# Performance work log

Measured on AMD Instinct MI355X. Metric: run time of the kernel, lower is better.

The kernel has to match this reference:

```python
import jax, jax.numpy as jnp
import numpy as np

N_AGENTS = 32
STATE_DIM = 6 * N_AGENTS      # 192
CONTROL_DIM = 3 * N_AGENTS    # 96
HIDDEN = 100
NEWTON_ITERS = 40

# Index maps from the cvxpy objective:
#   p[u_x_r]^T u[u_idx] + p[u_y_r]^T u[2*u_idx] + p[u_z_r]^T u[3*u_idx]
_u_idx = np.arange(N_AGENTS)
P_IDX = np.concatenate([3 * np.arange(1, N_AGENTS + 1),
                        4 * np.arange(1, N_AGENTS + 1),
                        5 * np.arange(1, N_AGENTS + 1)])
U_IDX = np.concatenate([_u_idx, 2 * _u_idx, 3 * _u_idx])


def _p_net(t, z, W1, b1, W2, b2, W3, b3):
    # DefaultPNet: MLP on concat([t, z]) with tanh hiddens (hidden_dim=100)
    x = jnp.concatenate([t, z], axis=-1)          # [B, 1+STATE_DIM]
    h = jnp.tanh(x @ W1 + b1)
    h = jnp.tanh(h @ W2 + b2)
    return h @ W3 + b3                            # [B, STATE_DIM]


def _solve_qp(q):
    # min_u q^T u + 0.5||u||^2 + 0.25||u||^4  (unconstrained, strictly convex)
    # Stationarity: q + (1+||u||^2) u = 0 => u = -q/(1+s), s = ||u||^2
    # => s (1+s)^2 = ||q||^2 ; solve scalar cubic per row via Newton.
    r = jnp.sum(q * q, axis=-1)                   # [B]
    s0 = jnp.cbrt(r)                              # good init: s ~ r^(1/3) for large r

    def step(s, _):
        one = 1.0 + s
        f = s * one * one - r
        fp = one * one + 2.0 * s * one
        return jnp.maximum(s - f / fp, 0.0), None

    s, _ = jax.lax.scan(step, s0, None, length=NEWTON_ITERS)
    return -q / (1.0 + s)[:, None]                # [B, CONTROL_DIM]


def setup_inputs() -> dict:
    key = jax.random.key(0)
    ks = jax.random.split(key, 8)
    B = 131072
    in_dim = 1 + STATE_DIM
    sc1 = 1.0 / np.sqrt(in_dim)
    sc2 = 1.0 / np.sqrt(HIDDEN)
    return {
        "z": jax.random.normal(ks[0], (B, STATE_DIM), jnp.float32),
        "t": jax.random.uniform(ks[1], (B, 1), jnp.float32),
        "W1": jax.random.normal(ks[2], (in_dim, HIDDEN), jnp.float32) * sc1,
        "b1": jnp.zeros((HIDDEN,), jnp.float32),
        "W2": jax.random.normal(ks[3], (HIDDEN, HIDDEN), jnp.float32) * sc2,
        "b2": jnp.zeros((HIDDEN,), jnp.float32),
        "W3": jax.random.normal(ks[4], (HIDDEN, STATE_DIM), jnp.float32) * sc2,
        "b3": jnp.zeros((STATE_DIM,), jnp.float32),
    }


def reference(z, t, W1, b1, W2, b2, W3, b3):
    p = _p_net(t, z, W1, b1, W2, b2, W3, b3)      # [B, STATE_DIM]
    # Accumulate linear coefficients onto u (indices overlap, so scatter-add)
    q = jnp.zeros((p.shape[0], CONTROL_DIM), p.dtype).at[:, U_IDX].add(p[:, P_IDX])
    return _solve_qp(q)                            # ustar [B, CONTROL_DIM]
```

## Files before the change

kernel.cpp:

```cpp
#include <hip/hip_runtime.h>
#include <hip/hip_bf16.h>


typedef __attribute__((ext_vector_type(8))) short short8;
typedef __attribute__((ext_vector_type(4))) short short4v;
typedef __attribute__((ext_vector_type(4))) float f32x4;

#define HST 116

__device__ __forceinline__ unsigned short f2bf(float f) {
  unsigned u = __float_as_uint(f);
  u += 0x7fffu + ((u >> 16) & 1u);
  return (unsigned short)(u >> 16);
}
__device__ __forceinline__ float tanh_fast(float x) {
  float ax = fabsf(x);
  float e = __builtin_amdgcn_exp2f(ax * -2.88539008177792681f);
  float r = (1.f - e) * __builtin_amdgcn_rcpf(1.f + e);
  return copysignf(r, x);
}

__global__ void cvx_prep(const float* __restrict__ W1, const float* __restrict__ b1,
                         const float* __restrict__ W2, const float* __restrict__ b2,
                         const float* __restrict__ W3, const float* __restrict__ b3,
                         short* __restrict__ pw) {
  int idx = blockIdx.x * 256 + threadIdx.x;

  if (idx < 21504) {
    int kt = idx / 3584, rem = idx % 3584;
    int nt = rem / 512, e = rem % 512;
    int lane = e >> 3, j = e & 7;
    int k = kt * 32 + (lane >> 4) * 8 + j;
    int n = nt * 16 + (lane & 15);
    float wv = (n < 100) ? W1[(k + 1) * 100 + n] : 0.f;
    pw[(kt * 7 + nt) * 512 + e] = (short)f2bf(wv);
    return;
  }
  idx -= 21504;
  if (idx < 14336) {
    int kt = idx / 3584, rem = idx % 3584;
    int nt = rem / 512, e = rem % 512;
    int lane = e >> 3, j = e & 7;
    int k = kt * 32 + (lane >> 4) * 8 + j;
    int n = nt * 16 + (lane & 15);
    float wv = (k < 100 && n < 100) ? W2[k * 100 + n] : 0.f;
    pw[21504 + (kt * 7 + nt) * 512 + e] = (short)f2bf(wv);
    return;
  }
  idx -= 14336;
  if (idx < 12288) {
    int kt = idx / 3072, rem = idx % 3072;
    int nt = rem / 512, e = rem % 512;
    int lane = e >> 3, j = e & 7;
    int k = kt * 32 + (lane >> 4) * 8 + j;
    int u = nt * 16 + (lane & 15);
    float wv = 0.f;
    if (k < 100) {
      const float* wr = W3 + k * 192;
      if (u <= 31) wv += wr[3 * u + 3];
      if ((u & 1) == 0 && u <= 62) wv += wr[2 * u + 4];
      if (u % 3 == 0 && u <= 93) wv += wr[(5 * u) / 3 + 5];
    }
    pw[35840 + (kt * 6 + nt) * 512 + e] = (short)f2bf(wv);
    return;
  }
  idx -= 12288;
  float* cb = (float*)(pw + 48128);
  if (idx < 112) { cb[idx] = (idx < 100) ? W1[idx] : 0.f; return; }
  idx -= 112;
  if (idx < 112) { cb[112 + idx] = (idx < 100) ? b1[idx] : 0.f; return; }
  idx -= 112;
  if (idx < 112) { cb[224 + idx] = (idx < 100) ? b2[idx] : 0.f; return; }
  idx -= 112;
  if (idx < 96) {
    int u = idx;
    float v = 0.f;
    if (u <= 31) v += b3[3 * u + 3];
    if ((u & 1) == 0 && u <= 62) v += b3[2 * u + 4];
    if (u % 3 == 0 && u <= 93) v += b3[(5 * u) / 3 + 5];
    cb[336 + u] = v;
  }
}

__global__ __launch_bounds__(512, 2) void cvx_main(
    const float* __restrict__ zin, const float* __restrict__ tin,
    const short* __restrict__ pw, float* __restrict__ out) {
  __shared__ __align__(16) short wbuf[48128];
  __shared__ __align__(16) short hbuf[8 * 32 * HST];

  const int tid = threadIdx.x;
  const int wid = tid >> 6;
  const int lane = tid & 63;
  const int l15 = lane & 15;
  const int qd = lane >> 4;

  for (int f = wid; f < 94; f += 8) {
    const short* g = pw + f * 512 + lane * 8;
    __builtin_amdgcn_global_load_lds(
        (const __attribute__((address_space(1))) void*)g,
        (__attribute__((address_space(3))) void*)&wbuf[f * 512], 16, 0, 0);
  }

  const float* cb = (const float*)(pw + 48128);
  float w0v[7], b1v[7], b2v[7], bqv[6];
#pragma unroll
  for (int nt = 0; nt < 7; nt++) {
    w0v[nt] = cb[nt * 16 + l15];
    b1v[nt] = cb[112 + nt * 16 + l15];
    b2v[nt] = cb[224 + nt * 16 + l15];
  }
#pragma unroll
  for (int nt = 0; nt < 6; nt++) bqv[nt] = cb[336 + nt * 16 + l15];

  const int row0 = blockIdx.x * 512 + wid * 32;
  const int hb = wid * 32 * HST;

  f32x4 zc[2][6][2];
  float tc[2];
#pragma unroll
  for (int mt = 0; mt < 2; mt++) {
    const float* zr = zin + (size_t)(row0 + mt * 16 + l15) * 192 + qd * 8;
#pragma unroll
    for (int kt = 0; kt < 6; kt++) {
      zc[mt][kt][0] = *(const f32x4*)(zr + kt * 32);
      zc[mt][kt][1] = *(const f32x4*)(zr + kt * 32 + 4);
    }
    tc[mt] = tin[row0 + mt * 16 + l15];
  }

  __syncthreads();

  auto ldh = [&](int off) -> short8 {
    short4v a = *(const short4v*)&hbuf[off];
    short4v b = *(const short4v*)&hbuf[off + 4];
    return __builtin_shufflevector(a, b, 0, 1, 2, 3, 4, 5, 6, 7);
  };

#pragma unroll 1
  for (int it = 0; it < 2; ++it) {
    const int rb = row0 + it * 256;

    short8 XA[2][6];
#pragma unroll
    for (int mt = 0; mt < 2; mt++)
#pragma unroll
      for (int kt = 0; kt < 6; kt++) {
        union { short8 s; __hip_bfloat162 h[4]; } u;
        f32x4 a = zc[mt][kt][0], b = zc[mt][kt][1];
        u.h[0] = __float22bfloat162_rn(make_float2(a[0], a[1]));
        u.h[1] = __float22bfloat162_rn(make_float2(a[2], a[3]));
        u.h[2] = __float22bfloat162_rn(make_float2(b[0], b[1]));
        u.h[3] = __float22bfloat162_rn(make_float2(b[2], b[3]));
        XA[mt][kt] = u.s;
      }
    float tv0 = tc[0], tv1 = tc[1];

    if (it == 0) {
#pragma unroll
      for (int mt = 0; mt < 2; mt++) {
        const float* zr = zin + (size_t)(row0 + 256 + mt * 16 + l15) * 192 + qd * 8;
#pragma unroll
        for (int kt = 0; kt < 6; kt++) {
          zc[mt][kt][0] = *(const f32x4*)(zr + kt * 32);
          zc[mt][kt][1] = *(const f32x4*)(zr + kt * 32 + 4);
        }
        tc[mt] = tin[row0 + 256 + mt * 16 + l15];
      }
    }

    f32x4 acc[2][7];
#pragma unroll
    for (int nt = 0; nt < 7; nt++) {
      f32x4 zzz = {0.f, 0.f, 0.f, 0.f};
      acc[0][nt] = zzz; acc[1][nt] = zzz;
    }
#pragma unroll
    for (int kt = 0; kt < 6; kt++)
#pragma unroll
      for (int nt = 0; nt < 7; nt++) {
        short8 bf = *(const short8*)&wbuf[(kt * 7 + nt) * 512 + lane * 8];
        acc[0][nt] = __builtin_amdgcn_mfma_f32_16x16x32_bf16(XA[0][kt], bf, acc[0][nt], 0, 0, 0);
        acc[1][nt] = __builtin_amdgcn_mfma_f32_16x16x32_bf16(XA[1][kt], bf, acc[1][nt], 0, 0, 0);
      }
    float tr[2][4];
#pragma unroll
    for (int r = 0; r < 4; r++) {
      tr[0][r] = __shfl(tv0, qd * 4 + r);
      tr[1][r] = __shfl(tv1, qd * 4 + r);
    }
#pragma unroll
    for (int mt = 0; mt < 2; mt++)
#pragma unroll
      for (int nt = 0; nt < 7; nt++)
#pragma unroll
        for (int r = 0; r < 4; r++) {
          float v = fmaf(tr[mt][r], w0v[nt], acc[mt][nt][r] + b1v[nt]);
          hbuf[hb + (mt * 16 + qd * 4 + r) * HST + nt * 16 + l15] = (short)f2bf(tanh_fast(v));
        }

    short8 HA[2][4];
#pragma unroll
    for (int mt = 0; mt < 2; mt++) {
      int ro = hb + (mt * 16 + l15) * HST;
#pragma unroll
      for (int kt = 0; kt < 3; kt++) HA[mt][kt] = ldh(ro + kt * 32 + qd * 8);
      HA[mt][3] = ldh(ro + 96 + (qd & 1) * 8);
    }
#pragma unroll
    for (int nt = 0; nt < 7; nt++) {
      f32x4 zzz = {0.f, 0.f, 0.f, 0.f};
      acc[0][nt] = zzz; acc[1][nt] = zzz;
    }
#pragma unroll
    for (int kt = 0; kt < 4; kt++)
#pragma unroll
      for (int nt = 0; nt < 7; nt++) {
        short8 bf = *(const short8*)&wbuf[(42 + kt * 7 + nt) * 512 + lane * 8];
        acc[0][nt] = __builtin_amdgcn_mfma_f32_16x16x32_bf16(HA[0][kt], bf, acc[0][nt], 0, 0, 0);
        acc[1][nt] = __builtin_amdgcn_mfma_f32_16x16x32_bf16(HA[1][kt], bf, acc[1][nt], 0, 0, 0);
      }
#pragma unroll
    for (int mt = 0; mt < 2; mt++)
#pragma unroll
      for (int nt = 0; nt < 7; nt++)
#pragma unroll
        for (int r = 0; r < 4; r++) {
          float v = acc[mt][nt][r] + b2v[nt];
          hbuf[hb + (mt * 16 + qd * 4 + r) * HST + nt * 16 + l15] = (short)f2bf(tanh_fast(v));
        }

#pragma unroll
    for (int mt = 0; mt < 2; mt++) {
      int ro = hb + (mt * 16 + l15) * HST;
#pragma unroll
      for (int kt = 0; kt < 3; kt++) HA[mt][kt] = ldh(ro + kt * 32 + qd * 8);
      HA[mt][3] = ldh(ro + 96 + (qd & 1) * 8);
    }
    f32x4 qa[2][6];
#pragma unroll
    for (int nt = 0; nt < 6; nt++) {
      f32x4 zzz = {0.f, 0.f, 0.f, 0.f};
      qa[0][nt] = zzz; qa[1][nt] = zzz;
    }
#pragma unroll
    for (int kt = 0; kt < 4; kt++)
#pragma unroll
      for (int nt = 0; nt < 6; nt++) {
        short8 bf = *(const short8*)&wbuf[(70 + kt * 6 + nt) * 512 + lane * 8];
        qa[0][nt] = __builtin_amdgcn_mfma_f32_16x16x32_bf16(HA[0][kt], bf, qa[0][nt], 0, 0, 0);
        qa[1][nt] = __builtin_amdgcn_mfma_f32_16x16x32_bf16(HA[1][kt], bf, qa[1][nt], 0, 0, 0);
      }

#pragma unroll
    for (int mt = 0; mt < 2; mt++) {
#pragma unroll
      for (int nt = 0; nt < 6; nt++) {
        float bq = bqv[nt];
        qa[mt][nt][0] += bq; qa[mt][nt][1] += bq;
        qa[mt][nt][2] += bq; qa[mt][nt][3] += bq;
      }
      f32x4 rs = {0.f, 0.f, 0.f, 0.f};
#pragma unroll
      for (int nt = 0; nt < 6; nt++) rs += qa[mt][nt] * qa[mt][nt];
      float rv[4];
#pragma unroll
      for (int r = 0; r < 4; r++) {
        float v = rs[r];
        v += __shfl_xor(v, 1);
        v += __shfl_xor(v, 2);
        v += __shfl_xor(v, 4);
        v += __shfl_xor(v, 8);
        rv[r] = v;
      }
      float r2 = rv[l15 & 3];
      float s = __builtin_amdgcn_exp2f(__builtin_amdgcn_logf(r2) * 0.333333333333f);
#pragma unroll
      for (int itn = 0; itn < 8; itn++) {
        float one = 1.f + s;
        float fv = fmaf(s * one, one, -r2);
        float fp = one * fmaf(2.f, s, one);
        s = fmaxf(s - fv * __builtin_amdgcn_rcpf(fp), 0.f);
      }
      float myinv = -__builtin_amdgcn_rcpf(1.f + s);
#pragma unroll
      for (int r = 0; r < 4; r++) {
        float inv = __shfl(myinv, (lane & 48) | r);
        float* orow = out + (size_t)(rb + mt * 16 + qd * 4 + r) * 96;
#pragma unroll
        for (int nt = 0; nt < 6; nt++)
          orow[nt * 16 + l15] = qa[mt][nt][r] * inv;
      }
    }
  }
}

extern "C" void kernel_launch(void* const* d_in, const int* in_sizes, int n_in,
                              void* d_out, int out_size, void* d_ws, size_t ws_size,
                              hipStream_t stream) {
  const float* z  = (const float*)d_in[0];
  const float* t  = (const float*)d_in[1];
  const float* W1 = (const float*)d_in[2];
  const float* b1 = (const float*)d_in[3];
  const float* W2 = (const float*)d_in[4];
  const float* b2 = (const float*)d_in[5];
  const float* W3 = (const float*)d_in[6];
  const float* b3 = (const float*)d_in[7];
  float* out = (float*)d_out;
  int B = in_sizes[0] / 192;

  short* pw = (short*)d_ws;
  cvx_prep<<<190, 256, 0, stream>>>(W1, b1, W2, b2, W3, b3, pw);
  cvx_main<<<B / 512, 512, 0, stream>>>(z, t, pw, out);
}
```

Measured before the change: 193.1 us.

## Double block size to 1024 threads with 16 rows per wave, biases in LDS

```diff
diff --git a/kernel.cpp b/kernel.cpp
--- a/kernel.cpp
+++ b/kernel.cpp
@@ -82,11 +82,12 @@
   }
 }
 
-__global__ __launch_bounds__(512, 2) void cvx_main(
+__global__ __launch_bounds__(1024, 4) void cvx_main(
     const float* __restrict__ zin, const float* __restrict__ tin,
     const short* __restrict__ pw, float* __restrict__ out) {
   __shared__ __align__(16) short wbuf[48128];
-  __shared__ __align__(16) short hbuf[8 * 32 * HST];
+  __shared__ __align__(16) short hbuf[16 * 16 * HST];
+  __shared__ __align__(16) float cbl[448];
 
   const int tid = threadIdx.x;
   const int wid = tid >> 6;
@@ -94,38 +95,27 @@
   const int l15 = lane & 15;
   const int qd = lane >> 4;
 
-  for (int f = wid; f < 94; f += 8) {
+  for (int f = wid; f < 94; f += 16) {
     const short* g = pw + f * 512 + lane * 8;
     __builtin_amdgcn_global_load_lds(
         (const __attribute__((address_space(1))) void*)g,
         (__attribute__((address_space(3))) void*)&wbuf[f * 512], 16, 0, 0);
   }
-
-  const float* cb = (const float*)(pw + 48128);
-  float w0v[7], b1v[7], b2v[7], bqv[6];
-#pragma unroll
-  for (int nt = 0; nt < 7; nt++) {
-    w0v[nt] = cb[nt * 16 + l15];
-    b1v[nt] = cb[112 + nt * 16 + l15];
-    b2v[nt] = cb[224 + nt * 16 + l15];
-  }
-#pragma unroll
-  for (int nt = 0; nt < 6; nt++) bqv[nt] = cb[336 + nt * 16 + l15];
-
-  const int row0 = blockIdx.x * 512 + wid * 32;
-  const int hb = wid * 32 * HST;
-
-  f32x4 zc[2][6][2];
-  float tc[2];
-#pragma unroll
-  for (int mt = 0; mt < 2; mt++) {
-    const float* zr = zin + (size_t)(row0 + mt * 16 + l15) * 192 + qd * 8;
+  if (tid < 448) cbl[tid] = ((const float*)(pw + 48128))[tid];
+
+  const int row0 = blockIdx.x * 512 + wid * 16;
+  const int hb = wid * 16 * HST;
+
+  f32x4 zc[6][2];
+  float tc;
+  {
+    const float* zr = zin + (size_t)(row0 + l15) * 192 + qd * 8;
 #pragma unroll
     for (int kt = 0; kt < 6; kt++) {
-      zc[mt][kt][0] = *(const f32x4*)(zr + kt * 32);
-      zc[mt][kt][1] = *(const f32x4*)(zr + kt * 32 + 4);
-    }
-    tc[mt] = tin[row0 + mt * 16 + l15];
+      zc[kt][0] = *(const f32x4*)(zr + kt * 32);
+      zc[kt][1] = *(const f32x4*)(zr + kt * 32 + 4);
+    }
+    tc = tin[row0 + l15];
   }
 
   __syncthreads();
@@ -140,156 +130,141 @@
   for (int it = 0; it < 2; ++it) {
     const int rb = row0 + it * 256;
 
-    short8 XA[2][6];
-#pragma unroll
-    for (int mt = 0; mt < 2; mt++)
+    short8 XA[6];
+#pragma unroll
+    for (int kt = 0; kt < 6; kt++) {
+      union { short8 s; __hip_bfloat162 h[4]; } u;
+      f32x4 a = zc[kt][0], b = zc[kt][1];
+      u.h[0] = __float22bfloat162_rn(make_float2(a[0], a[1]));
+      u.h[1] = __float22bfloat162_rn(make_float2(a[2], a[3]));
+      u.h[2] = __float22bfloat162_rn(make_float2(b[0], b[1]));
+      u.h[3] = __float22bfloat162_rn(make_float2(b[2], b[3]));
+      XA[kt] = u.s;
+    }
+    float tv = tc;
+
+    if (it == 0) {
+      const float* zr = zin + (size_t)(row0 + 256 + l15) * 192 + qd * 8;
 #pragma unroll
       for (int kt = 0; kt < 6; kt++) {
-        union { short8 s; __hip_bfloat162 h[4]; } u;
-        f32x4 a = zc[mt][kt][0], b = zc[mt][kt][1];
-        u.h[0] = __float22bfloat162_rn(make_float2(a[0], a[1]));
-        u.h[1] = __float22bfloat162_rn(make_float2(a[2], a[3]));
-        u.h[2] = __float22bfloat162_rn(make_float2(b[0], b[1]));
-        u.h[3] = __float22bfloat162_rn(make_float2(b[2], b[3]));
-        XA[mt][kt] = u.s;
-      }
-    float tv0 = tc[0], tv1 = tc[1];
-
-    if (it == 0) {
-#pragma unroll
-      for (int mt = 0; mt < 2; mt++) {
-        const float* zr = zin + (size_t)(row0 + 256 + mt * 16 + l15) * 192 + qd * 8;
-#pragma unroll
-        for (int kt = 0; kt < 6; kt++) {
-          zc[mt][kt][0] = *(const f32x4*)(zr + kt * 32);
-          zc[mt][kt][1] = *(const f32x4*)(zr + kt * 32 + 4);
-        }
-        tc[mt] = tin[row0 + 256 + mt * 16 + l15];
-      }
-    }
-
-    f32x4 acc[2][7];
+        zc[kt][0] = *(const f32x4*)(zr + kt * 32);
+        zc[kt][1] = *(const f32x4*)(zr + kt * 32 + 4);
+      }
+      tc = tin[row0 + 256 + l15];
+    }
+
+    f32x4 acc[7];
 #pragma unroll
     for (int nt = 0; nt < 7; nt++) {
       f32x4 zzz = {0.f, 0.f, 0.f, 0.f};
-      acc[0][nt] = zzz; acc[1][nt] = zzz;
+      acc[nt] = zzz;
     }
 #pragma unroll
     for (int kt = 0; kt < 6; kt++)
 #pragma unroll
       for (int nt = 0; nt < 7; nt++) {
         short8 bf = *(const short8*)&wbuf[(kt * 7 + nt) * 512 + lane * 8];
-        acc[0][nt] = __builtin_amdgcn_mfma_f32_16x16x32_bf16(XA[0][kt], bf, acc[0][nt], 0, 0, 0);
-        acc[1][nt] = __builtin_amdgcn_mfma_f32_16x16x32_bf16(XA[1][kt], bf, acc[1][nt], 0, 0, 0);
-      }
-    float tr[2][4];
-#pragma unroll
-    for (int r = 0; r < 4; r++) {
-      tr[0][r] = __shfl(tv0, qd * 4 + r);
-      tr[1][r] = __shfl(tv1, qd * 4 + r);
-    }
-#pragma unroll
-    for (int mt = 0; mt < 2; mt++)
-#pragma unroll
-      for (int nt = 0; nt < 7; nt++)
-#pragma unroll
-        for (int r = 0; r < 4; r++) {
-          float v = fmaf(tr[mt][r], w0v[nt], acc[mt][nt][r] + b1v[nt]);
-          hbuf[hb + (mt * 16 + qd * 4 + r) * HST + nt * 16 + l15] = (short)f2bf(tanh_fast(v));
-        }
-
-    short8 HA[2][4];
-#pragma unroll
-    for (int mt = 0; mt < 2; mt++) {
-      int ro = hb + (mt * 16 + l15) * HST;
-#pragma unroll
-      for (int kt = 0; kt < 3; kt++) HA[mt][kt] = ldh(ro + kt * 32 + qd * 8);
-      HA[mt][3] = ldh(ro + 96 + (qd & 1) * 8);
+        acc[nt] = __builtin_amdgcn_mfma_f32_16x16x32_bf16(XA[kt], bf, acc[nt], 0, 0, 0);
+      }
+    float tr[4];
+#pragma unroll
+    for (int r = 0; r < 4; r++) tr[r] = __shfl(tv, qd * 4 + r);
+#pragma unroll
+    for (int nt = 0; nt < 7; nt++) {
+      float w0v = cbl[nt * 16 + l15];
+      float b1v = cbl[112 + nt * 16 + l15];
+#pragma unroll
+      for (int r = 0; r < 4; r++) {
+        float v = fmaf(tr[r], w0v, acc[nt][r] + b1v);
+        hbuf[hb + (qd * 4 + r) * HST + nt * 16 + l15] = (short)f2bf(tanh_fast(v));
+      }
+    }
+
+    short8 HA[4];
+    {
+      int ro = hb + l15 * HST;
+#pragma unroll
+      for (int kt = 0; kt < 3; kt++) HA[kt] = ldh(ro + kt * 32 + qd * 8);
+      HA[3] = ldh(ro + 96 + (qd & 1) * 8);
     }
 #pragma unroll
     for (int nt = 0; nt < 7; nt++) {
       f32x4 zzz = {0.f, 0.f, 0.f, 0.f};
-      acc[0][nt] = zzz; acc[1][nt] = zzz;
+      acc[nt] = zzz;
     }
 #pragma unroll
     for (int kt = 0; kt < 4; kt++)
 #pragma unroll
       for (int nt = 0; nt < 7; nt++) {
         short8 bf = *(const short8*)&wbuf[(42 + kt * 7 + nt) * 512 + lane * 8];
-        acc[0][nt] = __builtin_amdgcn_mfma_f32_16x16x32_bf16(HA[0][kt], bf, acc[0][nt], 0, 0, 0);
-        acc[1][nt] = __builtin_amdgcn_mfma_f32_16x16x32_bf16(HA[1][kt], bf, acc[1][nt], 0, 0, 0);
-      }
-#pragma unroll
-    for (int mt = 0; mt < 2; mt++)
-#pragma unroll
-      for (int nt = 0; nt < 7; nt++)
-#pragma unroll
-        for (int r = 0; r < 4; r++) {
-          float v = acc[mt][nt][r] + b2v[nt];
-          hbuf[hb + (mt * 16 + qd * 4 + r) * HST + nt * 16 + l15] = (short)f2bf(tanh_fast(v));
-        }
-
-#pragma unroll
-    for (int mt = 0; mt < 2; mt++) {
-      int ro = hb + (mt * 16 + l15) * HST;
-#pragma unroll
-      for (int kt = 0; kt < 3; kt++) HA[mt][kt] = ldh(ro + kt * 32 + qd * 8);
-      HA[mt][3] = ldh(ro + 96 + (qd & 1) * 8);
-    }
-    f32x4 qa[2][6];
+        acc[nt] = __builtin_amdgcn_mfma_f32_16x16x32_bf16(HA[kt], bf, acc[nt], 0, 0, 0);
+      }
+#pragma unroll
+    for (int nt = 0; nt < 7; nt++) {
+      float b2v = cbl[224 + nt * 16 + l15];
+#pragma unroll
+      for (int r = 0; r < 4; r++) {
+        float v = acc[nt][r] + b2v;
+        hbuf[hb + (qd * 4 + r) * HST + nt * 16 + l15] = (short)f2bf(tanh_fast(v));
+      }
+    }
+
+    {
+      int ro = hb + l15 * HST;
+#pragma unroll
+      for (int kt = 0; kt < 3; kt++) HA[kt] = ldh(ro + kt * 32 + qd * 8);
+      HA[3] = ldh(ro + 96 + (qd & 1) * 8);
+    }
+    f32x4 qa[6];
 #pragma unroll
     for (int nt = 0; nt < 6; nt++) {
       f32x4 zzz = {0.f, 0.f, 0.f, 0.f};
-      qa[0][nt] = zzz; qa[1][nt] = zzz;
+      qa[nt] = zzz;
     }
 #pragma unroll
     for (int kt = 0; kt < 4; kt++)
 #pragma unroll
       for (int nt = 0; nt < 6; nt++) {
         short8 bf = *(const short8*)&wbuf[(70 + kt * 6 + nt) * 512 + lane * 8];
-        qa[0][nt] = __builtin_amdgcn_mfma_f32_16x16x32_bf16(HA[0][kt], bf, qa[0][nt], 0, 0, 0);
-        qa[1][nt] = __builtin_amdgcn_mfma_f32_16x16x32_bf16(HA[1][kt], bf, qa[1][nt], 0, 0, 0);
-      }
-
-#pragma unroll
-    for (int mt = 0; mt < 2; mt++) {
-#pragma unroll
-      for (int nt = 0; nt < 6; nt++) {
-        float bq = bqv[nt];
-        qa[mt][nt][0] += bq; qa[mt][nt][1] += bq;
-        qa[mt][nt][2] += bq; qa[mt][nt][3] += bq;
-      }
-      f32x4 rs = {0.f, 0.f, 0.f, 0.f};
-#pragma unroll
-      for (int nt = 0; nt < 6; nt++) rs += qa[mt][nt] * qa[mt][nt];
-      float rv[4];
-#pragma unroll
-      for (int r = 0; r < 4; r++) {
-        float v = rs[r];
-        v += __shfl_xor(v, 1);
-        v += __shfl_xor(v, 2);
-        v += __shfl_xor(v, 4);
-        v += __shfl_xor(v, 8);
-        rv[r] = v;
-      }
-      float r2 = rv[l15 & 3];
-      float s = __builtin_amdgcn_exp2f(__builtin_amdgcn_logf(r2) * 0.333333333333f);
-#pragma unroll
-      for (int itn = 0; itn < 8; itn++) {
-        float one = 1.f + s;
-        float fv = fmaf(s * one, one, -r2);
-        float fp = one * fmaf(2.f, s, one);
-        s = fmaxf(s - fv * __builtin_amdgcn_rcpf(fp), 0.f);
-      }
-      float myinv = -__builtin_amdgcn_rcpf(1.f + s);
-#pragma unroll
-      for (int r = 0; r < 4; r++) {
-        float inv = __shfl(myinv, (lane & 48) | r);
-        float* orow = out + (size_t)(rb + mt * 16 + qd * 4 + r) * 96;
-#pragma unroll
-        for (int nt = 0; nt < 6; nt++)
-          orow[nt * 16 + l15] = qa[mt][nt][r] * inv;
-      }
+        qa[nt] = __builtin_amdgcn_mfma_f32_16x16x32_bf16(HA[kt], bf, qa[nt], 0, 0, 0);
+      }
+
+#pragma unroll
+    for (int nt = 0; nt < 6; nt++) {
+      float bq = cbl[336 + nt * 16 + l15];
+      qa[nt][0] += bq; qa[nt][1] += bq;
+      qa[nt][2] += bq; qa[nt][3] += bq;
+    }
+    f32x4 rs = {0.f, 0.f, 0.f, 0.f};
+#pragma unroll
+    for (int nt = 0; nt < 6; nt++) rs += qa[nt] * qa[nt];
+    float rv[4];
+#pragma unroll
+    for (int r = 0; r < 4; r++) {
+      float v = rs[r];
+      v += __shfl_xor(v, 1);
+      v += __shfl_xor(v, 2);
+      v += __shfl_xor(v, 4);
+      v += __shfl_xor(v, 8);
+      rv[r] = v;
+    }
+    float r2 = rv[l15 & 3];
+    float s = __builtin_amdgcn_exp2f(__builtin_amdgcn_logf(r2) * 0.333333333333f);
+#pragma unroll
+    for (int itn = 0; itn < 8; itn++) {
+      float one = 1.f + s;
+      float fv = fmaf(s * one, one, -r2);
+      float fp = one * fmaf(2.f, s, one);
+      s = fmaxf(s - fv * __builtin_amdgcn_rcpf(fp), 0.f);
+    }
+    float myinv = -__builtin_amdgcn_rcpf(1.f + s);
+#pragma unroll
+    for (int r = 0; r < 4; r++) {
+      float inv = __shfl(myinv, (lane & 48) | r);
+      float* orow = out + (size_t)(rb + qd * 4 + r) * 96;
+#pragma unroll
+      for (int nt = 0; nt < 6; nt++)
+        orow[nt * 16 + l15] = qa[nt][r] * inv;
     }
   }
 }
@@ -310,5 +285,5 @@
 
   short* pw = (short*)d_ws;
   cvx_prep<<<190, 256, 0, stream>>>(W1, b1, W2, b2, W3, b3, pw);
-  cvx_main<<<B / 512, 512, 0, stream>>>(z, t, pw, out);
-}
+  cvx_main<<<B / 512, 1024, 0, stream>>>(z, t, pw, out);
+}
```

Result: slower. 266.9 us (+38.2%).

## Read MLP weight fragments directly from global memory instead of LDS staging

Applied to the files above, without the earlier changes.

```diff
diff --git a/kernel.cpp b/kernel.cpp
--- a/kernel.cpp
+++ b/kernel.cpp
@@ -82,10 +82,9 @@
   }
 }
 
-__global__ __launch_bounds__(512, 2) void cvx_main(
+__global__ __launch_bounds__(512, 4) void cvx_main(
     const float* __restrict__ zin, const float* __restrict__ tin,
     const short* __restrict__ pw, float* __restrict__ out) {
-  __shared__ __align__(16) short wbuf[48128];
   __shared__ __align__(16) short hbuf[8 * 32 * HST];
 
   const int tid = threadIdx.x;
@@ -94,13 +93,6 @@
   const int l15 = lane & 15;
   const int qd = lane >> 4;
 
-  for (int f = wid; f < 94; f += 8) {
-    const short* g = pw + f * 512 + lane * 8;
-    __builtin_amdgcn_global_load_lds(
-        (const __attribute__((address_space(1))) void*)g,
-        (__attribute__((address_space(3))) void*)&wbuf[f * 512], 16, 0, 0);
-  }
-
   const float* cb = (const float*)(pw + 48128);
   float w0v[7], b1v[7], b2v[7], bqv[6];
 #pragma unroll
@@ -112,8 +104,9 @@
 #pragma unroll
   for (int nt = 0; nt < 6; nt++) bqv[nt] = cb[336 + nt * 16 + l15];
 
-  const int row0 = blockIdx.x * 512 + wid * 32;
+  const int row0 = blockIdx.x * 256 + wid * 32;
   const int hb = wid * 32 * HST;
+  const short* wfrag = pw + lane * 8;
 
   f32x4 zc[2][6][2];
   float tc[2];
@@ -127,8 +120,6 @@
     }
     tc[mt] = tin[row0 + mt * 16 + l15];
   }
-
-  __syncthreads();
 
   auto ldh = [&](int off) -> short8 {
     short4v a = *(const short4v*)&hbuf[off];
@@ -136,160 +127,142 @@
     return __builtin_shufflevector(a, b, 0, 1, 2, 3, 4, 5, 6, 7);
   };
 
-#pragma unroll 1
-  for (int it = 0; it < 2; ++it) {
-    const int rb = row0 + it * 256;
-
-    short8 XA[2][6];
-#pragma unroll
-    for (int mt = 0; mt < 2; mt++)
-#pragma unroll
-      for (int kt = 0; kt < 6; kt++) {
-        union { short8 s; __hip_bfloat162 h[4]; } u;
-        f32x4 a = zc[mt][kt][0], b = zc[mt][kt][1];
-        u.h[0] = __float22bfloat162_rn(make_float2(a[0], a[1]));
-        u.h[1] = __float22bfloat162_rn(make_float2(a[2], a[3]));
-        u.h[2] = __float22bfloat162_rn(make_float2(b[0], b[1]));
-        u.h[3] = __float22bfloat162_rn(make_float2(b[2], b[3]));
-        XA[mt][kt] = u.s;
+  short8 XA[2][6];
+#pragma unroll
+  for (int mt = 0; mt < 2; mt++)
+#pragma unroll
+    for (int kt = 0; kt < 6; kt++) {
+      union { short8 s; __hip_bfloat162 h[4]; } u;
+      f32x4 a = zc[mt][kt][0], b = zc[mt][kt][1];
+      u.h[0] = __float22bfloat162_rn(make_float2(a[0], a[1]));
+      u.h[1] = __float22bfloat162_rn(make_float2(a[2], a[3]));
+      u.h[2] = __float22bfloat162_rn(make_float2(b[0], b[1]));
+      u.h[3] = __float22bfloat162_rn(make_float2(b[2], b[3]));
+      XA[mt][kt] = u.s;
+    }
+  float tv0 = tc[0], tv1 = tc[1];
+
+  f32x4 acc[2][7];
+#pragma unroll
+  for (int nt = 0; nt < 7; nt++) {
+    f32x4 zzz = {0.f, 0.f, 0.f, 0.f};
+    acc[0][nt] = zzz; acc[1][nt] = zzz;
+  }
+#pragma unroll
+  for (int kt = 0; kt < 6; kt++)
+#pragma unroll
+    for (int nt = 0; nt < 7; nt++) {
+      short8 bf = *(const short8*)(wfrag + (kt * 7 + nt) * 512);
+      acc[0][nt] = __builtin_amdgcn_mfma_f32_16x16x32_bf16(XA[0][kt], bf, acc[0][nt], 0, 0, 0);
+      acc[1][nt] = __builtin_amdgcn_mfma_f32_16x16x32_bf16(XA[1][kt], bf, acc[1][nt], 0, 0, 0);
+    }
+  float tr[2][4];
+#pragma unroll
+  for (int r = 0; r < 4; r++) {
+    tr[0][r] = __shfl(tv0, qd * 4 + r);
+    tr[1][r] = __shfl(tv1, qd * 4 + r);
+  }
+#pragma unroll
+  for (int mt = 0; mt < 2; mt++)
+#pragma unroll
+    for (int nt = 0; nt < 7; nt++)
+#pragma unroll
+      for (int r = 0; r < 4; r++) {
+        float v = fmaf(tr[mt][r], w0v[nt], acc[mt][nt][r] + b1v[nt]);
+        hbuf[hb + (mt * 16 + qd * 4 + r) * HST + nt * 16 + l15] = (short)f2bf(tanh_fast(v));
       }
-    float tv0 = tc[0], tv1 = tc[1];
-
-    if (it == 0) {
-#pragma unroll
-      for (int mt = 0; mt < 2; mt++) {
-        const float* zr = zin + (size_t)(row0 + 256 + mt * 16 + l15) * 192 + qd * 8;
-#pragma unroll
-        for (int kt = 0; kt < 6; kt++) {
-          zc[mt][kt][0] = *(const f32x4*)(zr + kt * 32);
-          zc[mt][kt][1] = *(const f32x4*)(zr + kt * 32 + 4);
-        }
-        tc[mt] = tin[row0 + 256 + mt * 16 + l15];
+
+  short8 HA[2][4];
+#pragma unroll
+  for (int mt = 0; mt < 2; mt++) {
+    int ro = hb + (mt * 16 + l15) * HST;
+#pragma unroll
+    for (int kt = 0; kt < 3; kt++) HA[mt][kt] = ldh(ro + kt * 32 + qd * 8);
+    HA[mt][3] = ldh(ro + 96 + (qd & 1) * 8);
+  }
+#pragma unroll
+  for (int nt = 0; nt < 7; nt++) {
+    f32x4 zzz = {0.f, 0.f, 0.f, 0.f};
+    acc[0][nt] = zzz; acc[1][nt] = zzz;
+  }
+#pragma unroll
+  for (int kt = 0; kt < 4; kt++)
+#pragma unroll
+    for (int nt = 0; nt < 7; nt++) {
+      short8 bf = *(const short8*)(wfrag + (42 + kt * 7 + nt) * 512);
+      acc[0][nt] = __builtin_amdgcn_mfma_f32_16x16x32_bf16(HA[0][kt], bf, acc[0][nt], 0, 0, 0);
+      acc[1][nt] = __builtin_amdgcn_mfma_f32_16x16x32_bf16(HA[1][kt], bf, acc[1][nt], 0, 0, 0);
+    }
+#pragma unroll
+  for (int mt = 0; mt < 2; mt++)
+#pragma unroll
+    for (int nt = 0; nt < 7; nt++)
+#pragma unroll
+      for (int r = 0; r < 4; r++) {
+        float v = acc[mt][nt][r] + b2v[nt];
+        hbuf[hb + (mt * 16 + qd * 4 + r) * HST + nt * 16 + l15] = (short)f2bf(tanh_fast(v));
       }
-    }
-
-    f32x4 acc[2][7];
-#pragma unroll
-    for (int nt = 0; nt < 7; nt++) {
-      f32x4 zzz = {0.f, 0.f, 0.f, 0.f};
-      acc[0][nt] = zzz; acc[1][nt] = zzz;
-    }
-#pragma unroll
-    for (int kt = 0; kt < 6; kt++)
-#pragma unroll
-      for (int nt = 0; nt < 7; nt++) {
-        short8 bf = *(const short8*)&wbuf[(kt * 7 + nt) * 512 + lane * 8];
-        acc[0][nt] = __builtin_amdgcn_mfma_f32_16x16x32_bf16(XA[0][kt], bf, acc[0][nt], 0, 0, 0);
-        acc[1][nt] = __builtin_amdgcn_mfma_f32_16x16x32_bf16(XA[1][kt], bf, acc[1][nt], 0, 0, 0);
-      }
-    float tr[2][4];
+
+#pragma unroll
+  for (int mt = 0; mt < 2; mt++) {
+    int ro = hb + (mt * 16 + l15) * HST;
+#pragma unroll
+    for (int kt = 0; kt < 3; kt++) HA[mt][kt] = ldh(ro + kt * 32 + qd * 8);
+    HA[mt][3] = ldh(ro + 96 + (qd & 1) * 8);
+  }
+  f32x4 qa[2][6];
+#pragma unroll
+  for (int nt = 0; nt < 6; nt++) {
+    f32x4 zzz = {0.f, 0.f, 0.f, 0.f};
+    qa[0][nt] = zzz; qa[1][nt] = zzz;
+  }
+#pragma unroll
+  for (int kt = 0; kt < 4; kt++)
+#pragma unroll
+    for (int nt = 0; nt < 6; nt++) {
+      short8 bf = *(const short8*)(wfrag + (70 + kt * 6 + nt) * 512);
+      qa[0][nt] = __builtin_amdgcn_mfma_f32_16x16x32_bf16(HA[0][kt], bf, qa[0][nt], 0, 0, 0);
+      qa[1][nt] = __builtin_amdgcn_mfma_f32_16x16x32_bf16(HA[1][kt], bf, qa[1][nt], 0, 0, 0);
+    }
+
+#pragma unroll
+  for (int mt = 0; mt < 2; mt++) {
+#pragma unroll
+    for (int nt = 0; nt < 6; nt++) {
+      float bq = bqv[nt];
+      qa[mt][nt][0] += bq; qa[mt][nt][1] += bq;
+      qa[mt][nt][2] += bq; qa[mt][nt][3] += bq;
+    }
+    f32x4 rs = {0.f, 0.f, 0.f, 0.f};
+#pragma unroll
+    for (int nt = 0; nt < 6; nt++) rs += qa[mt][nt] * qa[mt][nt];
+    float rv[4];
 #pragma unroll
     for (int r = 0; r < 4; r++) {
-      tr[0][r] = __shfl(tv0, qd * 4 + r);
-      tr[1][r] = __shfl(tv1, qd * 4 + r);
-    }
-#pragma unroll
-    for (int mt = 0; mt < 2; mt++)
-#pragma unroll
-      for (int nt = 0; nt < 7; nt++)
-#pragma unroll
-        for (int r = 0; r < 4; r++) {
-          float v = fmaf(tr[mt][r], w0v[nt], acc[mt][nt][r] + b1v[nt]);
-          hbuf[hb + (mt * 16 + qd * 4 + r) * HST + nt * 16 + l15] = (short)f2bf(tanh_fast(v));
-        }
-
-    short8 HA[2][4];
-#pragma unroll
-    for (int mt = 0; mt < 2; mt++) {
-      int ro = hb + (mt * 16 + l15) * HST;
-#pragma unroll
-      for (int kt = 0; kt < 3; kt++) HA[mt][kt] = ldh(ro + kt * 32 + qd * 8);
-      HA[mt][3] = ldh(ro + 96 + (qd & 1) * 8);
-    }
-#pragma unroll
-    for (int nt = 0; nt < 7; nt++) {
-      f32x4 zzz = {0.f, 0.f, 0.f, 0.f};
-      acc[0][nt] = zzz; acc[1][nt] = zzz;
-    }
-#pragma unroll
-    for (int kt = 0; kt < 4; kt++)
-#pragma unroll
-      for (int nt = 0; nt < 7; nt++) {
-        short8 bf = *(const short8*)&wbuf[(42 + kt * 7 + nt) * 512 + lane * 8];
-        acc[0][nt] = __builtin_amdgcn_mfma_f32_16x16x32_bf16(HA[0][kt], bf, acc[0][nt], 0, 0, 0);
-        acc[1][nt] = __builtin_amdgcn_mfma_f32_16x16x32_bf16(HA[1][kt], bf, acc[1][nt], 0, 0, 0);
-      }
-#pragma unroll
-    for (int mt = 0; mt < 2; mt++)
-#pragma unroll
-      for (int nt = 0; nt < 7; nt++)
-#pragma unroll
-        for (int r = 0; r < 4; r++) {
-          float v = acc[mt][nt][r] + b2v[nt];
-          hbuf[hb + (mt * 16 + qd * 4 + r) * HST + nt * 16 + l15] = (short)f2bf(tanh_fast(v));
-        }
-
-#pragma unroll
-    for (int mt = 0; mt < 2; mt++) {
-      int ro = hb + (mt * 16 + l15) * HST;
-#pragma unroll
-      for (int kt = 0; kt < 3; kt++) HA[mt][kt] = ldh(ro + kt * 32 + qd * 8);
-      HA[mt][3] = ldh(ro + 96 + (qd & 1) * 8);
-    }
-    f32x4 qa[2][6];
-#pragma unroll
-    for (int nt = 0; nt < 6; nt++) {
-      f32x4 zzz = {0.f, 0.f, 0.f, 0.f};
-      qa[0][nt] = zzz; qa[1][nt] = zzz;
-    }
-#pragma unroll
-    for (int kt = 0; kt < 4; kt++)
-#pragma unroll
-      for (int nt = 0; nt < 6; nt++) {
-        short8 bf = *(const short8*)&wbuf[(70 + kt * 6 + nt) * 512 + lane * 8];
-        qa[0][nt] = __builtin_amdgcn_mfma_f32_16x16x32_bf16(HA[0][kt], bf, qa[0][nt], 0, 0, 0);
-        qa[1][nt] = __builtin_amdgcn_mfma_f32_16x16x32_bf16(HA[1][kt], bf, qa[1][nt], 0, 0, 0);
-      }
-
-#pragma unroll
-    for (int mt = 0; mt < 2; mt++) {
-#pragma unroll
-      for (int nt = 0; nt < 6; nt++) {
-        float bq = bqv[nt];
-        qa[mt][nt][0] += bq; qa[mt][nt][1] += bq;
-        qa[mt][nt][2] += bq; qa[mt][nt][3] += bq;
-      }
-      f32x4 rs = {0.f, 0.f, 0.f, 0.f};
-#pragma unroll
-      for (int nt = 0; nt < 6; nt++) rs += qa[mt][nt] * qa[mt][nt];
-      float rv[4];
-#pragma unroll
-      for (int r = 0; r < 4; r++) {
-        float v = rs[r];
-        v += __shfl_xor(v, 1);
-        v += __shfl_xor(v, 2);
-        v += __shfl_xor(v, 4);
-        v += __shfl_xor(v, 8);
-        rv[r] = v;
-      }
-      float r2 = rv[l15 & 3];
-      float s = __builtin_amdgcn_exp2f(__builtin_amdgcn_logf(r2) * 0.333333333333f);
-#pragma unroll
-      for (int itn = 0; itn < 8; itn++) {
-        float one = 1.f + s;
-        float fv = fmaf(s * one, one, -r2);
-        float fp = one * fmaf(2.f, s, one);
-        s = fmaxf(s - fv * __builtin_amdgcn_rcpf(fp), 0.f);
-      }
-      float myinv = -__builtin_amdgcn_rcpf(1.f + s);
-#pragma unroll
-      for (int r = 0; r < 4; r++) {
-        float inv = __shfl(myinv, (lane & 48) | r);
-        float* orow = out + (size_t)(rb + mt * 16 + qd * 4 + r) * 96;
-#pragma unroll
-        for (int nt = 0; nt < 6; nt++)
-          orow[nt * 16 + l15] = qa[mt][nt][r] * inv;
-      }
+      float v = rs[r];
+      v += __shfl_xor(v, 1);
+      v += __shfl_xor(v, 2);
+      v += __shfl_xor(v, 4);
+      v += __shfl_xor(v, 8);
+      rv[r] = v;
+    }
+    float r2 = rv[l15 & 3];
+    float s = __builtin_amdgcn_exp2f(__builtin_amdgcn_logf(r2) * 0.333333333333f);
+#pragma unroll
+    for (int itn = 0; itn < 8; itn++) {
+      float one = 1.f + s;
+      float fv = fmaf(s * one, one, -r2);
+      float fp = one * fmaf(2.f, s, one);
+      s = fmaxf(s - fv * __builtin_amdgcn_rcpf(fp), 0.f);
+    }
+    float myinv = -__builtin_amdgcn_rcpf(1.f + s);
+#pragma unroll
+    for (int r = 0; r < 4; r++) {
+      float inv = __shfl(myinv, (lane & 48) | r);
+      float* orow = out + (size_t)(row0 + mt * 16 + qd * 4 + r) * 96;
+#pragma unroll
+      for (int nt = 0; nt < 6; nt++)
+        orow[nt * 16 + l15] = qa[mt][nt][r] * inv;
     }
   }
 }
@@ -310,5 +283,5 @@
 
   short* pw = (short*)d_ws;
   cvx_prep<<<190, 256, 0, stream>>>(W1, b1, W2, b2, W3, b3, pw);
-  cvx_main<<<B / 512, 512, 0, stream>>>(z, t, pw, out);
-}
+  cvx_main<<<B / 256, 512, 0, stream>>>(z, t, pw, out);
+}
```

New measurement: 199.2 us. +3.1%, slower.

## Stream next-tile z prefetch in chunks across layer-1 MFMAs, move biases to LDS

Applied to the files above, without the earlier changes.

```diff
diff --git a/kernel.cpp b/kernel.cpp
--- a/kernel.cpp
+++ b/kernel.cpp
@@ -18,6 +18,14 @@
   float e = __builtin_amdgcn_exp2f(ax * -2.88539008177792681f);
   float r = (1.f - e) * __builtin_amdgcn_rcpf(1.f + e);
   return copysignf(r, x);
+}
+__device__ __forceinline__ short8 pack_bf8(f32x4 a, f32x4 b) {
+  union { short8 s; __hip_bfloat162 h[4]; } u;
+  u.h[0] = __float22bfloat162_rn(make_float2(a[0], a[1]));
+  u.h[1] = __float22bfloat162_rn(make_float2(a[2], a[3]));
+  u.h[2] = __float22bfloat162_rn(make_float2(b[0], b[1]));
+  u.h[3] = __float22bfloat162_rn(make_float2(b[2], b[3]));
+  return u.s;
 }
 
 __global__ void cvx_prep(const float* __restrict__ W1, const float* __restrict__ b1,
@@ -87,6 +95,7 @@
     const short* __restrict__ pw, float* __restrict__ out) {
   __shared__ __align__(16) short wbuf[48128];
   __shared__ __align__(16) short hbuf[8 * 32 * HST];
+  __shared__ __align__(16) float cbl[448];
 
   const int tid = threadIdx.x;
   const int wid = tid >> 6;
@@ -100,33 +109,25 @@
         (const __attribute__((address_space(1))) void*)g,
         (__attribute__((address_space(3))) void*)&wbuf[f * 512], 16, 0, 0);
   }
-
-  const float* cb = (const float*)(pw + 48128);
-  float w0v[7], b1v[7], b2v[7], bqv[6];
-#pragma unroll
-  for (int nt = 0; nt < 7; nt++) {
-    w0v[nt] = cb[nt * 16 + l15];
-    b1v[nt] = cb[112 + nt * 16 + l15];
-    b2v[nt] = cb[224 + nt * 16 + l15];
-  }
-#pragma unroll
-  for (int nt = 0; nt < 6; nt++) bqv[nt] = cb[336 + nt * 16 + l15];
+  if (tid < 448) cbl[tid] = ((const float*)(pw + 48128))[tid];
 
   const int row0 = blockIdx.x * 512 + wid * 32;
   const int hb = wid * 32 * HST;
 
-  f32x4 zc[2][6][2];
-  float tc[2];
+  short8 XA[2][6];
+  float tc0, tc1;
 #pragma unroll
   for (int mt = 0; mt < 2; mt++) {
     const float* zr = zin + (size_t)(row0 + mt * 16 + l15) * 192 + qd * 8;
 #pragma unroll
     for (int kt = 0; kt < 6; kt++) {
-      zc[mt][kt][0] = *(const f32x4*)(zr + kt * 32);
-      zc[mt][kt][1] = *(const f32x4*)(zr + kt * 32 + 4);
-    }
-    tc[mt] = tin[row0 + mt * 16 + l15];
-  }
+      f32x4 a = *(const f32x4*)(zr + kt * 32);
+      f32x4 b = *(const f32x4*)(zr + kt * 32 + 4);
+      XA[mt][kt] = pack_bf8(a, b);
+    }
+  }
+  tc0 = tin[row0 + l15];
+  tc1 = tin[row0 + 16 + l15];
 
   __syncthreads();
 
@@ -136,37 +137,12 @@
     return __builtin_shufflevector(a, b, 0, 1, 2, 3, 4, 5, 6, 7);
   };
 
+  short8 XN[2][6];
+  float tn0, tn1;
+
 #pragma unroll 1
-  for (int it = 0; it < 2; ++it) {
-    const int rb = row0 + it * 256;
-
-    short8 XA[2][6];
-#pragma unroll
-    for (int mt = 0; mt < 2; mt++)
-#pragma unroll
-      for (int kt = 0; kt < 6; kt++) {
-        union { short8 s; __hip_bfloat162 h[4]; } u;
-        f32x4 a = zc[mt][kt][0], b = zc[mt][kt][1];
-        u.h[0] = __float22bfloat162_rn(make_float2(a[0], a[1]));
-        u.h[1] = __float22bfloat162_rn(make_float2(a[2], a[3]));
-        u.h[2] = __float22bfloat162_rn(make_float2(b[0], b[1]));
-        u.h[3] = __float22bfloat162_rn(make_float2(b[2], b[3]));
-        XA[mt][kt] = u.s;
-      }
-    float tv0 = tc[0], tv1 = tc[1];
-
-    if (it == 0) {
-#pragma unroll
-      for (int mt = 0; mt < 2; mt++) {
-        const float* zr = zin + (size_t)(row0 + 256 + mt * 16 + l15) * 192 + qd * 8;
-#pragma unroll
-        for (int kt = 0; kt < 6; kt++) {
-          zc[mt][kt][0] = *(const f32x4*)(zr + kt * 32);
-          zc[mt][kt][1] = *(const f32x4*)(zr + kt * 32 + 4);
-        }
-        tc[mt] = tin[row0 + 256 + mt * 16 + l15];
-      }
-    }
+  for (int ii = 0; ii < 2; ++ii) {
+    const int rb = row0 + ii * 256;
 
     f32x4 acc[2][7];
 #pragma unroll
@@ -174,29 +150,108 @@
       f32x4 zzz = {0.f, 0.f, 0.f, 0.f};
       acc[0][nt] = zzz; acc[1][nt] = zzz;
     }
-#pragma unroll
-    for (int kt = 0; kt < 6; kt++)
+
+    f32x4 sg[2][2][2];
+    const float* zb = zin + (size_t)(row0 + 256 + l15) * 192 + qd * 8;
+
+    if (ii == 0) {
+#pragma unroll
+      for (int mt = 0; mt < 2; mt++)
+#pragma unroll
+        for (int kp = 0; kp < 2; kp++) {
+          sg[mt][kp][0] = *(const f32x4*)(zb + mt * 3072 + kp * 32);
+          sg[mt][kp][1] = *(const f32x4*)(zb + mt * 3072 + kp * 32 + 4);
+        }
+      __builtin_amdgcn_sched_barrier(0);
+    }
+
+#pragma unroll
+    for (int kt = 0; kt < 2; kt++)
 #pragma unroll
       for (int nt = 0; nt < 7; nt++) {
         short8 bf = *(const short8*)&wbuf[(kt * 7 + nt) * 512 + lane * 8];
         acc[0][nt] = __builtin_amdgcn_mfma_f32_16x16x32_bf16(XA[0][kt], bf, acc[0][nt], 0, 0, 0);
         acc[1][nt] = __builtin_amdgcn_mfma_f32_16x16x32_bf16(XA[1][kt], bf, acc[1][nt], 0, 0, 0);
       }
+
+    if (ii == 0) {
+#pragma unroll
+      for (int mt = 0; mt < 2; mt++)
+#pragma unroll
+        for (int kp = 0; kp < 2; kp++)
+          XN[mt][kp] = pack_bf8(sg[mt][kp][0], sg[mt][kp][1]);
+#pragma unroll
+      for (int mt = 0; mt < 2; mt++)
+#pragma unroll
+        for (int kp = 0; kp < 2; kp++) {
+          sg[mt][kp][0] = *(const f32x4*)(zb + mt * 3072 + (2 + kp) * 32);
+          sg[mt][kp][1] = *(const f32x4*)(zb + mt * 3072 + (2 + kp) * 32 + 4);
+        }
+      __builtin_amdgcn_sched_barrier(0);
+    }
+
+#pragma unroll
+    for (int kt = 2; kt < 4; kt++)
+#pragma unroll
+      for (int nt = 0; nt < 7; nt++) {
+        short8 bf = *(const short8*)&wbuf[(kt * 7 + nt) * 512 + lane * 8];
+        acc[0][nt] = __builtin_amdgcn_mfma_f32_16x16x32_bf16(XA[0][kt], bf, acc[0][nt], 0, 0, 0);
+        acc[1][nt] = __builtin_amdgcn_mfma_f32_16x16x32_bf16(XA[1][kt], bf, acc[1][nt], 0, 0, 0);
+      }
+
+    if (ii == 0) {
+#pragma unroll
+      for (int mt = 0; mt < 2; mt++)
+#pragma unroll
+        for (int kp = 0; kp < 2; kp++)
+          XN[mt][2 + kp] = pack_bf8(sg[mt][kp][0], sg[mt][kp][1]);
+#pragma unroll
+      for (int mt = 0; mt < 2; mt++)
+#pragma unroll
+        for (int kp = 0; kp < 2; kp++) {
+          sg[mt][kp][0] = *(const f32x4*)(zb + mt * 3072 + (4 + kp) * 32);
+          sg[mt][kp][1] = *(const f32x4*)(zb + mt * 3072 + (4 + kp) * 32 + 4);
+        }
+      tn0 = tin[row0 + 256 + l15];
+      tn1 = tin[row0 + 256 + 16 + l15];
+      __builtin_amdgcn_sched_barrier(0);
+    }
+
+#pragma unroll
+    for (int kt = 4; kt < 6; kt++)
+#pragma unroll
+      for (int nt = 0; nt < 7; nt++) {
+        short8 bf = *(const short8*)&wbuf[(kt * 7 + nt) * 512 + lane * 8];
+        acc[0][nt] = __builtin_amdgcn_mfma_f32_16x16x32_bf16(XA[0][kt], bf, acc[0][nt], 0, 0, 0);
+        acc[1][nt] = __builtin_amdgcn_mfma_f32_16x16x32_bf16(XA[1][kt], bf, acc[1][nt], 0, 0, 0);
+      }
+
     float tr[2][4];
 #pragma unroll
     for (int r = 0; r < 4; r++) {
-      tr[0][r] = __shfl(tv0, qd * 4 + r);
-      tr[1][r] = __shfl(tv1, qd * 4 + r);
-    }
-#pragma unroll
-    for (int mt = 0; mt < 2; mt++)
-#pragma unroll
-      for (int nt = 0; nt < 7; nt++)
+      tr[0][r] = __shfl(tc0, qd * 4 + r);
+      tr[1][r] = __shfl(tc1, qd * 4 + r);
+    }
+#pragma unroll
+    for (int nt = 0; nt < 7; nt++) {
+      float w0v = cbl[nt * 16 + l15];
+      float b1v = cbl[112 + nt * 16 + l15];
+#pragma unroll
+      for (int mt = 0; mt < 2; mt++)
 #pragma unroll
         for (int r = 0; r < 4; r++) {
-          float v = fmaf(tr[mt][r], w0v[nt], acc[mt][nt][r] + b1v[nt]);
+          float v = fmaf(tr[mt][r], w0v, acc[mt][nt][r] + b1v);
           hbuf[hb + (mt * 16 + qd * 4 + r) * HST + nt * 16 + l15] = (short)f2bf(tanh_fast(v));
         }
+    }
+
+    if (ii == 0) {
+#pragma unroll
+      for (int mt = 0; mt < 2; mt++)
+#pragma unroll
+        for (int kp = 0; kp < 2; kp++)
+          XN[mt][4 + kp] = pack_bf8(sg[mt][kp][0], sg[mt][kp][1]);
+    }
 
     short8 HA[2][4];
 #pragma unroll
@@ -220,14 +275,16 @@
         acc[1][nt] = __builtin_amdgcn_mfma_f32_16x16x32_bf16(HA[1][kt], bf, acc[1][nt], 0, 0, 0);
       }
 #pragma unroll
-    for (int mt = 0; mt < 2; mt++)
-#pragma unroll
-      for (int nt = 0; nt < 7; nt++)
+    for (int nt = 0; nt < 7; nt++) {
+      float b2v = cbl[224 + nt * 16 + l15];
+#pragma unroll
+      for (int mt = 0; mt < 2; mt++)
 #pragma unroll
         for (int r = 0; r < 4; r++) {
-          float v = acc[mt][nt][r] + b2v[nt];
+          float v = acc[mt][nt][r] + b2v;
           hbuf[hb + (mt * 16 + qd * 4 + r) * HST + nt * 16 + l15] = (short)f2bf(tanh_fast(v));
         }
+    }
 
 #pragma unroll
     for (int mt = 0; mt < 2; mt++) {
@@ -255,7 +312,7 @@
     for (int mt = 0; mt < 2; mt++) {
 #pragma unroll
       for (int nt = 0; nt < 6; nt++) {
-        float bq = bqv[nt];
+        float bq = cbl[336 + nt * 16 + l15];
         qa[mt][nt][0] += bq; qa[mt][nt][1] += bq;
         qa[mt][nt][2] += bq; qa[mt][nt][3] += bq;
       }
@@ -290,6 +347,14 @@
         for (int nt = 0; nt < 6; nt++)
           orow[nt * 16 + l15] = qa[mt][nt][r] * inv;
       }
+    }
+
+    if (ii == 0) {
+#pragma unroll
+      for (int mt = 0; mt < 2; mt++)
+#pragma unroll
+        for (int kt = 0; kt < 6; kt++) XA[mt][kt] = XN[mt][kt];
+      tc0 = tn0; tc1 = tn1;
     }
   }
 }
```

Result: no change. 190.7 us (-1.3%).
